# Performance work log

Hardware: AMD Instinct MI355X
Metric: run time of the kernel (lower is better)

## Reference

```python
import jax, jax.numpy as jnp
import numpy as np

D_IN = 1024
D_OUT = 1024
NUM_HEADS = 16
HEAD_DIM = D_OUT // NUM_HEADS


def setup_inputs() -> dict:
    key = jax.random.key(0)
    ks = jax.random.split(key, 6)
    scale = 0.02
    x = jax.random.normal(ks[0], (4, 2048, D_IN), dtype=jnp.float32)
    Wq = jax.random.normal(ks[1], (D_IN, D_OUT), dtype=jnp.float32) * scale
    Wk = jax.random.normal(ks[2], (D_IN, D_OUT), dtype=jnp.float32) * scale
    Wv = jax.random.normal(ks[3], (D_IN, D_OUT), dtype=jnp.float32) * scale
    Wo = jax.random.normal(ks[4], (D_OUT, D_OUT), dtype=jnp.float32) * scale
    bo = jax.random.normal(ks[5], (D_OUT,), dtype=jnp.float32) * scale
    return {"x": x, "Wq": Wq, "Wk": Wk, "Wv": Wv, "Wo": Wo, "bo": bo}


def reference(x, Wq, Wk, Wv, Wo, bo):
    b, n, _ = x.shape
    # QKV projections -> [b, h, n, hd]
    def split_heads(t):
        return t.reshape(b, n, NUM_HEADS, HEAD_DIM).transpose(0, 2, 1, 3)
    q = split_heads(x @ Wq)
    k = split_heads(x @ Wk)
    v = split_heads(x @ Wv)
    # scaled causal attention scores [b, h, n, n]
    scores = jnp.einsum('bhqd,bhkd->bhqk', q, k) / jnp.sqrt(jnp.float32(HEAD_DIM))
    causal = jnp.tril(jnp.ones((n, n), dtype=bool))
    scores = jnp.where(causal, scores, -jnp.inf)
    attn = jax.nn.softmax(scores, axis=-1)
    # dropout p=0.0 -> identity
    ctx = jnp.einsum('bhqk,bhkd->bhqd', attn, v)  # [b, h, n, hd]
    ctx = ctx.transpose(0, 2, 1, 3).reshape(b, n, D_OUT)
    return ctx @ Wo + bo
```

## Files before the change

kernel.cpp:

```cpp
#include <hip/hip_runtime.h>
#include <hip/hip_bf16.h>

typedef __bf16 bf16;
typedef __attribute__((ext_vector_type(8))) __bf16 bf16x8;
typedef __attribute__((ext_vector_type(4))) __bf16 bf16x4;
typedef __attribute__((ext_vector_type(4))) float floatx4;

#define DM 1024
#define NH 16
#define HD 64
#define SEQ 2048
#define BATCH 4
#define MTOT (BATCH * SEQ)

#if __has_builtin(__builtin_amdgcn_exp2f)
#define EXP2(x) __builtin_amdgcn_exp2f(x)
#else
#define EXP2(x) exp2f(x)
#endif

#define GLDS(g, l) \
  __builtin_amdgcn_global_load_lds((const __attribute__((address_space(1))) void*)(g), \
                                   (__attribute__((address_space(3))) void*)(l), 16, 0, 0)

__global__ void prep(const float* __restrict__ x,
                     const float* __restrict__ Wq, const float* __restrict__ Wk,
                     const float* __restrict__ Wv, const float* __restrict__ Wo,
                     bf16* __restrict__ xb, bf16* __restrict__ Wqkvt, bf16* __restrict__ Wot) {
  __shared__ float tile[32][33];
  int bid = blockIdx.x, tid = threadIdx.x;
  if (bid < 8192) {
    int i = bid * 256 + tid;
    float4 v = ((const float4*)x)[i];
    bf16x4 o;
    o[0] = (bf16)v.x; o[1] = (bf16)v.y; o[2] = (bf16)v.z; o[3] = (bf16)v.w;
    ((bf16x4*)xb)[i] = o;
    return;
  }
  int b2 = bid - 8192;
  int z = b2 >> 10, t = b2 & 1023;
  const float* W;
  bf16* Wt;
  if (z == 0) { W = Wq; Wt = Wqkvt; }
  else if (z == 1) { W = Wk; Wt = Wqkvt + (size_t)DM * DM; }
  else if (z == 2) { W = Wv; Wt = Wqkvt + (size_t)2 * DM * DM; }
  else { W = Wo; Wt = Wot; }
  int n0 = (t & 31) * 32, k0 = (t >> 5) * 32;
  int tx = tid & 31, ty = tid >> 5;
#pragma unroll
  for (int j = 0; j < 32; j += 8)
    tile[ty + j][tx] = W[(size_t)(k0 + ty + j) * DM + n0 + tx];
  __syncthreads();
#pragma unroll
  for (int j = 0; j < 32; j += 8)
    Wt[(size_t)(n0 + ty + j) * DM + k0 + tx] = (bf16)tile[tx][ty + j];
}

#define BK 64

__global__ __launch_bounds__(256, 3) void gemm_qkv(const bf16* __restrict__ A,
                                                   const bf16* __restrict__ Bt,
                                                   bf16* __restrict__ Qb,
                                                   bf16* __restrict__ Kb,
                                                   bf16* __restrict__ Vt) {
  __shared__ __align__(16) bf16 Alds[128 * BK];
  __shared__ __align__(16) bf16 Blds[128 * BK];
  const int K = 1024;
  int m0 = blockIdx.x * 128;
  int n0 = blockIdx.y * 128;
  int tid = threadIdx.x;
  int wave = tid >> 6, lane = tid & 63;
  int wm = (wave & 1) * 64, wn = (wave >> 1) * 64;
  int lm = lane & 15, quad = lane >> 4;
  int lm7 = lm & 7;

  int cbase = wave * 64 + lane;
  const bf16* gA[4];
  const bf16* gB[4];
  bf16 *lA[4], *lB[4];
#pragma unroll
  for (int seg = 0; seg < 4; ++seg) {
    int c = seg * 256 + cbase;
    int row = c >> 3;
    int col8 = (c & 7) ^ (row & 7);
    gA[seg] = A + (size_t)(m0 + row) * K + col8 * 8;
    gB[seg] = Bt + (size_t)(n0 + row) * K + col8 * 8;
    lA[seg] = Alds + c * 8;
    lB[seg] = Blds + c * 8;
  }

  floatx4 acc[4][4] = {};
  for (int kt = 0; kt < K; kt += BK) {
    __syncthreads();
#pragma unroll
    for (int seg = 0; seg < 4; ++seg) {
      GLDS(gA[seg] + kt, lA[seg]);
      GLDS(gB[seg] + kt, lB[seg]);
    }
    __syncthreads();
#pragma unroll
    for (int ks = 0; ks < 2; ++ks) {
      int xk = (ks * 4 + quad) ^ lm7;
      bf16x8 af[4], bfr[4];
#pragma unroll
      for (int t = 0; t < 4; ++t) {
        af[t] = *(const bf16x8*)(Alds + (wm + t * 16 + lm) * BK + xk * 8);
        bfr[t] = *(const bf16x8*)(Blds + (wn + t * 16 + lm) * BK + xk * 8);
      }
#pragma unroll
      for (int i = 0; i < 4; ++i)
#pragma unroll
        for (int j = 0; j < 4; ++j)
          acc[i][j] = __builtin_amdgcn_mfma_f32_16x16x32_bf16(af[i], bfr[j], acc[i][j], 0, 0, 0);
    }
  }

  int proj = n0 >> 10;
  if (proj == 2) {
#pragma unroll
    for (int i = 0; i < 4; ++i) {
      int Rb = m0 + wm + i * 16 + quad * 4;
      int b = Rb >> 11, nb = Rb & 2047;
#pragma unroll
      for (int j = 0; j < 4; ++j) {
        int cc = (n0 + wn + j * 16 + lm) & 1023;
        int h = cc >> 6, d = cc & 63;
        bf16x4 ov;
#pragma unroll
        for (int r = 0; r < 4; ++r) ov[r] = (bf16)acc[i][j][r];
        *(bf16x4*)(Vt + ((size_t)(b * NH + h) * HD + d) * SEQ + nb) = ov;
      }
    }
  } else {
    bf16* P = proj ? Kb : Qb;
#pragma unroll
    for (int i = 0; i < 4; ++i) {
#pragma unroll
      for (int j = 0; j < 4; ++j) {
        int cc = (n0 + wn + j * 16 + lm) & 1023;
        int h = cc >> 6, d = cc & 63;
#pragma unroll
        for (int r = 0; r < 4; ++r) {
          int R = m0 + wm + i * 16 + quad * 4 + r;
          int b = R >> 11, n = R & 2047;
          P[((size_t)(b * NH + h) * SEQ + n) * HD + d] = (bf16)acc[i][j][r];
        }
      }
    }
  }
}

__global__ __launch_bounds__(256, 3) void gemm_out(const bf16* __restrict__ A,
                                                   const bf16* __restrict__ Bt,
                                                   const float* __restrict__ bias,
                                                   float* __restrict__ out) {
  __shared__ __align__(16) bf16 Alds[128 * BK];
  __shared__ __align__(16) bf16 Blds[128 * BK];
  const int K = 1024;
  int m0 = blockIdx.x * 128;
  int n0 = blockIdx.y * 128;
  int tid = threadIdx.x;
  int wave = tid >> 6, lane = tid & 63;
  int wm = (wave & 1) * 64, wn = (wave >> 1) * 64;
  int lm = lane & 15, quad = lane >> 4;
  int lm7 = lm & 7;

  int cbase = wave * 64 + lane;
  const bf16* gA[4];
  const bf16* gB[4];
  bf16 *lA[4], *lB[4];
#pragma unroll
  for (int seg = 0; seg < 4; ++seg) {
    int c = seg * 256 + cbase;
    int row = c >> 3;
    int col8 = (c & 7) ^ (row & 7);
    gA[seg] = A + (size_t)(m0 + row) * K + col8 * 8;
    gB[seg] = Bt + (size_t)(n0 + row) * K + col8 * 8;
    lA[seg] = Alds + c * 8;
    lB[seg] = Blds + c * 8;
  }

  floatx4 acc[4][4] = {};
  for (int kt = 0; kt < K; kt += BK) {
    __syncthreads();
#pragma unroll
    for (int seg = 0; seg < 4; ++seg) {
      GLDS(gA[seg] + kt, lA[seg]);
      GLDS(gB[seg] + kt, lB[seg]);
    }
    __syncthreads();
#pragma unroll
    for (int ks = 0; ks < 2; ++ks) {
      int xk = (ks * 4 + quad) ^ lm7;
      bf16x8 af[4], bfr[4];
#pragma unroll
      for (int t = 0; t < 4; ++t) {
        af[t] = *(const bf16x8*)(Alds + (wm + t * 16 + lm) * BK + xk * 8);
        bfr[t] = *(const bf16x8*)(Blds + (wn + t * 16 + lm) * BK + xk * 8);
      }
#pragma unroll
      for (int i = 0; i < 4; ++i)
#pragma unroll
        for (int j = 0; j < 4; ++j)
          acc[i][j] = __builtin_amdgcn_mfma_f32_16x16x32_bf16(af[i], bfr[j], acc[i][j], 0, 0, 0);
    }
  }
#pragma unroll
  for (int i = 0; i < 4; ++i)
#pragma unroll
    for (int j = 0; j < 4; ++j)
#pragma unroll
      for (int r = 0; r < 4; ++r) {
        int R = m0 + wm + i * 16 + quad * 4 + r;
        int C = n0 + wn + j * 16 + lm;
        out[(size_t)R * DM + C] = acc[i][j][r] + bias[C];
      }
}

__global__ __launch_bounds__(512, 2) void attn(const bf16* __restrict__ Qb,
                                               const bf16* __restrict__ Kb,
                                               const bf16* __restrict__ Vt,
                                               bf16* __restrict__ ctx) {
  __shared__ __align__(16) bf16 KV[32768];
  int blk = blockIdx.x;
  int xcd = blk & 7;
  int idx = blk >> 3;
  int bh = (idx & 7) * 8 + xcd;
  int pr = idx >> 3;
  int tid = threadIdx.x, wave = tid >> 6, lane = tid & 63;
  int qg = wave & 3, par = wave >> 2;
  int lm = lane & 15, quad = lane >> 4;
  int lm7 = lm & 7;
  const bf16* Qp = Qb + (size_t)bh * SEQ * HD;
  const bf16* Kp = Kb + (size_t)bh * SEQ * HD;
  const bf16* Vp = Vt + (size_t)bh * HD * SEQ;
  int b = bh >> 4, h = bh & 15;
  const float QSCALE = 0.125f * 1.4426950408889634f;

  int c = tid;
  int r = c >> 3, l = (c & 7) ^ (r & 7);
  const bf16* Kg = Kp + (size_t)r * HD + l * 8;
  const bf16* Vg = Vp + (size_t)r * SEQ + (l >> 2) * 32 + (l & 3) * 4;

  int kread = par * 4096;
  int vread = 8192 + par * 4096;

  bf16x8 ones;
#pragma unroll
  for (int j = 0; j < 8; ++j) ones[j] = (lm == 0) ? (bf16)1.0f : (bf16)0.0f;

  int xk0 = (quad ^ lm7) * 8;
  int xk1 = ((4 + quad) ^ lm7) * 8;

  float* cbuf = (float*)&KV[0];
  int cb = qg * 2176 + lane;

#pragma unroll 1
  for (int half = 0; half < 2; ++half) {
    int qt = half ? pr : 15 - pr;
    int q0 = qt * 128;
    int rowbase = q0 + qg * 32;
    int ns = qt + 1;

    bf16x8 qfA[2], qfB[2];
#pragma unroll
    for (int ks2 = 0; ks2 < 2; ++ks2) {
      bf16x8 qa = *(const bf16x8*)(Qp + (size_t)(rowbase + lm) * HD + ks2 * 32 + quad * 8);
      bf16x8 qb = *(const bf16x8*)(Qp + (size_t)(rowbase + 16 + lm) * HD + ks2 * 32 + quad * 8);
#pragma unroll
      for (int j = 0; j < 8; ++j) {
        qa[j] = (bf16)((float)qa[j] * QSCALE);
        qb[j] = (bf16)((float)qb[j] * QSCALE);
      }
      qfA[ks2] = qa;
      qfB[ks2] = qb;
    }

    floatx4 accA[4] = {}, accB[4] = {};
    floatx4 aclA = {}, aclB = {};

    if (half) __syncthreads();

    bf16x8 kr0 = *(const bf16x8*)(Kg);
    bf16x8 kr1 = *(const bf16x8*)(Kg + (size_t)64 * HD);
    bf16x4 v0a = *(const bf16x4*)(Vg),      v0b = *(const bf16x4*)(Vg + 16);
    bf16x4 v1a = *(const bf16x4*)(Vg + 64), v1b = *(const bf16x4*)(Vg + 80);
    *(bf16x8*)(KV + c * 8) = kr0;
    *(bf16x8*)(KV + 4096 + c * 8) = kr1;
    *(bf16x4*)(KV + 8192 + c * 8) = v0a;  *(bf16x4*)(KV + 8192 + c * 8 + 4) = v0b;
    *(bf16x4*)(KV + 12288 + c * 8) = v1a; *(bf16x4*)(KV + 12288 + c * 8 + 4) = v1b;

#pragma unroll 1
    for (int s = 0; s < ns; ++s) {
      __syncthreads();
      int bofs = (s & 1) << 14;
      int nofs = bofs ^ 16384;
      bool pf = (s + 1 < ns);
      if (pf) {
        int kt = (2 * s + 2) * 64;
        kr0 = *(const bf16x8*)(Kg + (size_t)kt * HD);
        kr1 = *(const bf16x8*)(Kg + (size_t)(kt + 64) * HD);
        v0a = *(const bf16x4*)(Vg + kt);      v0b = *(const bf16x4*)(Vg + kt + 16);
        v1a = *(const bf16x4*)(Vg + kt + 64); v1b = *(const bf16x4*)(Vg + kt + 80);
      }
      int kv0 = (2 * s + par) * 64;

      if (kv0 <= rowbase + 31) {
        const bf16* Kl = KV + bofs + kread;
        const bf16* Vl = KV + bofs + vread;
        floatx4 stA[4] = {}, stB[4] = {};
#pragma unroll
        for (int mt = 0; mt < 4; ++mt) {
          const bf16* kr = Kl + (mt * 16 + lm) * 64;
          bf16x8 kf0 = *(const bf16x8*)(kr + xk0);
          bf16x8 kf1 = *(const bf16x8*)(kr + xk1);
          stA[mt] = __builtin_amdgcn_mfma_f32_16x16x32_bf16(kf0, qfA[0], stA[mt], 0, 0, 0);
          stA[mt] = __builtin_amdgcn_mfma_f32_16x16x32_bf16(kf1, qfA[1], stA[mt], 0, 0, 0);
          stB[mt] = __builtin_amdgcn_mfma_f32_16x16x32_bf16(kf0, qfB[0], stB[mt], 0, 0, 0);
          stB[mt] = __builtin_amdgcn_mfma_f32_16x16x32_bf16(kf1, qfB[1], stB[mt], 0, 0, 0);
        }

        bf16x8 pfA2[2], pfB2[2];
        if (kv0 + 63 <= rowbase) {
#pragma unroll
          for (int mt = 0; mt < 4; ++mt)
#pragma unroll
            for (int rr = 0; rr < 4; ++rr) {
              pfA2[mt >> 1][(mt & 1) * 4 + rr] = (bf16)EXP2(stA[mt][rr]);
              pfB2[mt >> 1][(mt & 1) * 4 + rr] = (bf16)EXP2(stB[mt][rr]);
            }
        } else {
          int qrelA = rowbase - kv0 + lm;
          int qrelB = qrelA + 16;
#pragma unroll
          for (int mt = 0; mt < 4; ++mt)
#pragma unroll
            for (int rr = 0; rr < 4; ++rr) {
              int kvrel = mt * 16 + quad * 4 + rr;
              float pa = EXP2(stA[mt][rr]);
              float pbv = EXP2(stB[mt][rr]);
              if (kvrel > qrelA) pa = 0.f;
              if (kvrel > qrelB) pbv = 0.f;
              pfA2[mt >> 1][(mt & 1) * 4 + rr] = (bf16)pa;
              pfB2[mt >> 1][(mt & 1) * 4 + rr] = (bf16)pbv;
            }
        }

#pragma unroll
        for (int ks = 0; ks < 2; ++ks) {
          int xv = ks ? xk1 : xk0;
          aclA = __builtin_amdgcn_mfma_f32_16x16x32_bf16(ones, pfA2[ks], aclA, 0, 0, 0);
          aclB = __builtin_amdgcn_mfma_f32_16x16x32_bf16(ones, pfB2[ks], aclB, 0, 0, 0);
#pragma unroll
          for (int db = 0; db < 4; ++db) {
            bf16x8 vf = *(const bf16x8*)(Vl + (db * 16 + lm) * 64 + xv);
            accA[db] = __builtin_amdgcn_mfma_f32_16x16x32_bf16(vf, pfA2[ks], accA[db], 0, 0, 0);
            accB[db] = __builtin_amdgcn_mfma_f32_16x16x32_bf16(vf, pfB2[ks], accB[db], 0, 0, 0);
          }
        }
      }

      if (pf) {
        *(bf16x8*)(KV + nofs + c * 8) = kr0;
        *(bf16x8*)(KV + nofs + 4096 + c * 8) = kr1;
        *(bf16x4*)(KV + nofs + 8192 + c * 8) = v0a;  *(bf16x4*)(KV + nofs + 8192 + c * 8 + 4) = v0b;
        *(bf16x4*)(KV + nofs + 12288 + c * 8) = v1a; *(bf16x4*)(KV + nofs + 12288 + c * 8 + 4) = v1b;
      }
    }

    __syncthreads();
    if (par) {
#pragma unroll
      for (int db = 0; db < 4; ++db)
#pragma unroll
        for (int rr = 0; rr < 4; ++rr) {
          cbuf[cb + (db * 4 + rr) * 64] = accA[db][rr];
          cbuf[cb + (17 + db * 4 + rr) * 64] = accB[db][rr];
        }
      cbuf[cb + 16 * 64] = aclA[0];
      cbuf[cb + 33 * 64] = aclB[0];
    }
    __syncthreads();
    if (!par) {
      float aA = aclA[0] + cbuf[cb + 16 * 64];
      float aB = aclB[0] + cbuf[cb + 33 * 64];
#pragma unroll
      for (int db = 0; db < 4; ++db)
#pragma unroll
        for (int rr = 0; rr < 4; ++rr) {
          accA[db][rr] += cbuf[cb + (db * 4 + rr) * 64];
          accB[db][rr] += cbuf[cb + (17 + db * 4 + rr) * 64];
        }

      float linvA = 1.0f / __shfl(aA, lm, 64);
      float linvB = 1.0f / __shfl(aB, lm, 64);

      bf16* crowA = ctx + ((size_t)b * SEQ + rowbase + lm) * DM + h * 64;
      bf16* crowB = crowA + (size_t)16 * DM;
#pragma unroll
      for (int db = 0; db < 4; ++db) {
        bf16x4 oa, ob;
#pragma unroll
        for (int rr = 0; rr < 4; ++rr) {
          oa[rr] = (bf16)(accA[db][rr] * linvA);
          ob[rr] = (bf16)(accB[db][rr] * linvB);
        }
        *(bf16x4*)(crowA + db * 16 + quad * 4) = oa;
        *(bf16x4*)(crowB + db * 16 + quad * 4) = ob;
      }
    }
  }
}

extern "C" void kernel_launch(void* const* d_in, const int* in_sizes, int n_in,
                              void* d_out, int out_size, void* d_ws, size_t ws_size,
                              hipStream_t stream) {
  const float* x = (const float*)d_in[0];
  const float* Wq = (const float*)d_in[1];
  const float* Wk = (const float*)d_in[2];
  const float* Wv = (const float*)d_in[3];
  const float* Wo = (const float*)d_in[4];
  const float* bo = (const float*)d_in[5];
  float* out = (float*)d_out;

  bf16* ws = (bf16*)d_ws;
  bf16* xb = ws;
  bf16* Wqkvt = xb + (size_t)MTOT * DM;
  bf16* Wot = Wqkvt + (size_t)3 * DM * DM;
  bf16* Qb = Wot + (size_t)DM * DM;
  bf16* Kb = Qb + (size_t)BATCH * NH * SEQ * HD;
  bf16* Vtb = Kb + (size_t)BATCH * NH * SEQ * HD;
  bf16* ctx = xb;

  prep<<<8192 + 4096, 256, 0, stream>>>(x, Wq, Wk, Wv, Wo, xb, Wqkvt, Wot);
  gemm_qkv<<<dim3(MTOT / 128, 3 * DM / 128), 256, 0, stream>>>(xb, Wqkvt, Qb, Kb, Vtb);
  attn<<<512, 512, 0, stream>>>(Qb, Kb, Vtb, ctx);
  gemm_out<<<dim3(MTOT / 128, DM / 128), 256, 0, stream>>>(ctx, Wot, bo, out);
}
```

Measured before the change: 220.5 us.

## Read K and V directly from global memory in attention, dropping LDS staging

```diff
diff --git a/kernel.cpp b/kernel.cpp
--- a/kernel.cpp
+++ b/kernel.cpp
@@ -221,7 +221,7 @@
                                                const bf16* __restrict__ Kb,
                                                const bf16* __restrict__ Vt,
                                                bf16* __restrict__ ctx) {
-  __shared__ __align__(16) bf16 KV[32768];
+  __shared__ float cbuf[8704];
   int blk = blockIdx.x;
   int xcd = blk & 7;
   int idx = blk >> 3;
@@ -230,29 +230,16 @@
   int tid = threadIdx.x, wave = tid >> 6, lane = tid & 63;
   int qg = wave & 3, par = wave >> 2;
   int lm = lane & 15, quad = lane >> 4;
-  int lm7 = lm & 7;
   const bf16* Qp = Qb + (size_t)bh * SEQ * HD;
   const bf16* Kp = Kb + (size_t)bh * SEQ * HD;
   const bf16* Vp = Vt + (size_t)bh * HD * SEQ;
   int b = bh >> 4, h = bh & 15;
   const float QSCALE = 0.125f * 1.4426950408889634f;
 
-  int c = tid;
-  int r = c >> 3, l = (c & 7) ^ (r & 7);
-  const bf16* Kg = Kp + (size_t)r * HD + l * 8;
-  const bf16* Vg = Vp + (size_t)r * SEQ + (l >> 2) * 32 + (l & 3) * 4;
-
-  int kread = par * 4096;
-  int vread = 8192 + par * 4096;
-
   bf16x8 ones;
 #pragma unroll
   for (int j = 0; j < 8; ++j) ones[j] = (lm == 0) ? (bf16)1.0f : (bf16)0.0f;
 
-  int xk0 = (quad ^ lm7) * 8;
-  int xk1 = ((4 + quad) ^ lm7) * 8;
-
-  float* cbuf = (float*)&KV[0];
   int cb = qg * 2176 + lane;
 
 #pragma unroll 1
@@ -261,6 +248,9 @@
     int q0 = qt * 128;
     int rowbase = q0 + qg * 32;
     int ns = qt + 1;
+    int tb = rowbase + 31 - par * 64;
+    int nsw = tb < 0 ? 0 : (tb >> 7) + 1;
+    if (nsw > ns) nsw = ns;
 
     bf16x8 qfA[2], qfB[2];
 #pragma unroll
@@ -281,90 +271,61 @@
 
     if (half) __syncthreads();
 
-    bf16x8 kr0 = *(const bf16x8*)(Kg);
-    bf16x8 kr1 = *(const bf16x8*)(Kg + (size_t)64 * HD);
-    bf16x4 v0a = *(const bf16x4*)(Vg),      v0b = *(const bf16x4*)(Vg + 16);
-    bf16x4 v1a = *(const bf16x4*)(Vg + 64), v1b = *(const bf16x4*)(Vg + 80);
-    *(bf16x8*)(KV + c * 8) = kr0;
-    *(bf16x8*)(KV + 4096 + c * 8) = kr1;
-    *(bf16x4*)(KV + 8192 + c * 8) = v0a;  *(bf16x4*)(KV + 8192 + c * 8 + 4) = v0b;
-    *(bf16x4*)(KV + 12288 + c * 8) = v1a; *(bf16x4*)(KV + 12288 + c * 8 + 4) = v1b;
-
 #pragma unroll 1
-    for (int s = 0; s < ns; ++s) {
-      __syncthreads();
-      int bofs = (s & 1) << 14;
-      int nofs = bofs ^ 16384;
-      bool pf = (s + 1 < ns);
-      if (pf) {
-        int kt = (2 * s + 2) * 64;
-        kr0 = *(const bf16x8*)(Kg + (size_t)kt * HD);
-        kr1 = *(const bf16x8*)(Kg + (size_t)(kt + 64) * HD);
-        v0a = *(const bf16x4*)(Vg + kt);      v0b = *(const bf16x4*)(Vg + kt + 16);
-        v1a = *(const bf16x4*)(Vg + kt + 64); v1b = *(const bf16x4*)(Vg + kt + 80);
-      }
+    for (int s = 0; s < nsw; ++s) {
       int kv0 = (2 * s + par) * 64;
 
-      if (kv0 <= rowbase + 31) {
-        const bf16* Kl = KV + bofs + kread;
-        const bf16* Vl = KV + bofs + vread;
-        floatx4 stA[4] = {}, stB[4] = {};
-#pragma unroll
-        for (int mt = 0; mt < 4; ++mt) {
-          const bf16* kr = Kl + (mt * 16 + lm) * 64;
-          bf16x8 kf0 = *(const bf16x8*)(kr + xk0);
-          bf16x8 kf1 = *(const bf16x8*)(kr + xk1);
-          stA[mt] = __builtin_amdgcn_mfma_f32_16x16x32_bf16(kf0, qfA[0], stA[mt], 0, 0, 0);
-          stA[mt] = __builtin_amdgcn_mfma_f32_16x16x32_bf16(kf1, qfA[1], stA[mt], 0, 0, 0);
-          stB[mt] = __builtin_amdgcn_mfma_f32_16x16x32_bf16(kf0, qfB[0], stB[mt], 0, 0, 0);
-          stB[mt] = __builtin_amdgcn_mfma_f32_16x16x32_bf16(kf1, qfB[1], stB[mt], 0, 0, 0);
+      floatx4 stA[4] = {}, stB[4] = {};
+#pragma unroll
+      for (int mt = 0; mt < 4; ++mt) {
+        const bf16* kr = Kp + (size_t)(kv0 + mt * 16 + lm) * HD + quad * 8;
+        bf16x8 kf0 = *(const bf16x8*)(kr);
+        bf16x8 kf1 = *(const bf16x8*)(kr + 32);
+        stA[mt] = __builtin_amdgcn_mfma_f32_16x16x32_bf16(kf0, qfA[0], stA[mt], 0, 0, 0);
+        stA[mt] = __builtin_amdgcn_mfma_f32_16x16x32_bf16(kf1, qfA[1], stA[mt], 0, 0, 0);
+        stB[mt] = __builtin_amdgcn_mfma_f32_16x16x32_bf16(kf0, qfB[0], stB[mt], 0, 0, 0);
+        stB[mt] = __builtin_amdgcn_mfma_f32_16x16x32_bf16(kf1, qfB[1], stB[mt], 0, 0, 0);
+      }
+
+      bf16x8 pfA2[2], pfB2[2];
+      if (kv0 + 63 <= rowbase) {
+#pragma unroll
+        for (int mt = 0; mt < 4; ++mt)
+#pragma unroll
+          for (int rr = 0; rr < 4; ++rr) {
+            pfA2[mt >> 1][(mt & 1) * 4 + rr] = (bf16)EXP2(stA[mt][rr]);
+            pfB2[mt >> 1][(mt & 1) * 4 + rr] = (bf16)EXP2(stB[mt][rr]);
+          }
+      } else {
+        int qrelA = rowbase - kv0 + lm;
+        int qrelB = qrelA + 16;
+#pragma unroll
+        for (int mt = 0; mt < 4; ++mt)
+#pragma unroll
+          for (int rr = 0; rr < 4; ++rr) {
+            int kvrel = mt * 16 + quad * 4 + rr;
+            float pa = EXP2(stA[mt][rr]);
+            float pbv = EXP2(stB[mt][rr]);
+            if (kvrel > qrelA) pa = 0.f;
+            if (kvrel > qrelB) pbv = 0.f;
+            pfA2[mt >> 1][(mt & 1) * 4 + rr] = (bf16)pa;
+            pfB2[mt >> 1][(mt & 1) * 4 + rr] = (bf16)pbv;
+          }
+      }
+
+#pragma unroll
+      for (int ks = 0; ks < 2; ++ks) {
+        aclA = __builtin_amdgcn_mfma_f32_16x16x32_bf16(ones, pfA2[ks], aclA, 0, 0, 0);
+        aclB = __builtin_amdgcn_mfma_f32_16x16x32_bf16(ones, pfB2[ks], aclB, 0, 0, 0);
+#pragma unroll
+        for (int db = 0; db < 4; ++db) {
+          const bf16* vr = Vp + (size_t)(db * 16 + lm) * SEQ + kv0 + ks * 32 + quad * 4;
+          bf16x4 v0 = *(const bf16x4*)(vr);
+          bf16x4 v1 = *(const bf16x4*)(vr + 16);
+          bf16x8 vf = __builtin_shufflevector(v0, v1, 0, 1, 2, 3, 4, 5, 6, 7);
+          accA[db] = __builtin_amdgcn_mfma_f32_16x16x32_bf16(vf, pfA2[ks], accA[db], 0, 0, 0);
+          accB[db] = __builtin_amdgcn_mfma_f32_16x16x32_bf16(vf, pfB2[ks], accB[db], 0, 0, 0);
         }
-
-        bf16x8 pfA2[2], pfB2[2];
-        if (kv0 + 63 <= rowbase) {
-#pragma unroll
-          for (int mt = 0; mt < 4; ++mt)
-#pragma unroll
-            for (int rr = 0; rr < 4; ++rr) {
-              pfA2[mt >> 1][(mt & 1) * 4 + rr] = (bf16)EXP2(stA[mt][rr]);
-              pfB2[mt >> 1][(mt & 1) * 4 + rr] = (bf16)EXP2(stB[mt][rr]);
-            }
-        } else {
-          int qrelA = rowbase - kv0 + lm;
-          int qrelB = qrelA + 16;
-#pragma unroll
-          for (int mt = 0; mt < 4; ++mt)
-#pragma unroll
-            for (int rr = 0; rr < 4; ++rr) {
-              int kvrel = mt * 16 + quad * 4 + rr;
-              float pa = EXP2(stA[mt][rr]);
-              float pbv = EXP2(stB[mt][rr]);
-              if (kvrel > qrelA) pa = 0.f;
-              if (kvrel > qrelB) pbv = 0.f;
-              pfA2[mt >> 1][(mt & 1) * 4 + rr] = (bf16)pa;
-              pfB2[mt >> 1][(mt & 1) * 4 + rr] = (bf16)pbv;
-            }
-        }
-
-#pragma unroll
-        for (int ks = 0; ks < 2; ++ks) {
-          int xv = ks ? xk1 : xk0;
-          aclA = __builtin_amdgcn_mfma_f32_16x16x32_bf16(ones, pfA2[ks], aclA, 0, 0, 0);
-          aclB = __builtin_amdgcn_mfma_f32_16x16x32_bf16(ones, pfB2[ks], aclB, 0, 0, 0);
-#pragma unroll
-          for (int db = 0; db < 4; ++db) {
-            bf16x8 vf = *(const bf16x8*)(Vl + (db * 16 + lm) * 64 + xv);
-            accA[db] = __builtin_amdgcn_mfma_f32_16x16x32_bf16(vf, pfA2[ks], accA[db], 0, 0, 0);
-            accB[db] = __builtin_amdgcn_mfma_f32_16x16x32_bf16(vf, pfB2[ks], accB[db], 0, 0, 0);
-          }
-        }
-      }
-
-      if (pf) {
-        *(bf16x8*)(KV + nofs + c * 8) = kr0;
-        *(bf16x8*)(KV + nofs + 4096 + c * 8) = kr1;
-        *(bf16x4*)(KV + nofs + 8192 + c * 8) = v0a;  *(bf16x4*)(KV + nofs + 8192 + c * 8 + 4) = v0b;
-        *(bf16x4*)(KV + nofs + 12288 + c * 8) = v1a; *(bf16x4*)(KV + nofs + 12288 + c * 8 + 4) = v1b;
       }
     }
 
```

Measured after the change: 360.2 us. +63.4%, slower.
